# Kernel optimization log

Measured on AMD Instinct MI355X. Metric: run time of the kernel, lower is better.

Reference implementation:

```python
import jax, jax.numpy as jnp
import numpy as np

B, N, D, F, L, R = 16, 1024, 256, 128, 2, 2


def setup_inputs() -> dict:
    key = jax.random.key(0)
    ks = jax.random.split(key, 12)
    s = 0.05
    return {
        "node_embed": jax.random.normal(ks[0], (B, N, D), jnp.float32),
        "input_x": jax.random.normal(ks[1], (B, F), jnp.float32),
        "adj": jax.random.randint(ks[2], (R, B, N, N), 0, 2, jnp.int32),
        "WQi_w": jax.random.normal(ks[3], (L, F, F), jnp.float32) * s,
        "WQi_b": jnp.zeros((L, F), jnp.float32),
        "WQ_w": jax.random.normal(ks[4], (L, D + F, D), jnp.float32) * s,
        "WQ_b": jnp.zeros((L, D), jnp.float32),
        "WK_w": jax.random.normal(ks[5], (L, R, D + F, D), jnp.float32) * s,
        "WK_b": jnp.zeros((L, R, D), jnp.float32),
        "WV_w": jax.random.normal(ks[6], (L, R, D + F, D), jnp.float32) * s,
        "WV_b": jnp.zeros((L, R, D), jnp.float32),
        "WF_w": jax.random.normal(ks[7], (L, R * D, D), jnp.float32) * s,
        "WF_b": jnp.zeros((L, D), jnp.float32),
        "ln_g": jnp.ones((L, D), jnp.float32),
        "ln_b": jnp.zeros((L, D), jnp.float32),
    }


def _layer_norm(x, g, b, eps=1e-5):
    mu = jnp.mean(x, axis=-1, keepdims=True)
    var = jnp.var(x, axis=-1, keepdims=True)
    return (x - mu) * jax.lax.rsqrt(var + eps) * g + b


def reference(node_embed, input_x, adj, WQi_w, WQi_b, WQ_w, WQ_b,
              WK_w, WK_b, WV_w, WV_b, WF_w, WF_b, ln_g, ln_b):
    scale = 1.0 / (D ** 0.5)
    h = node_embed
    for l in range(L):
        # input feature projection, broadcast over nodes
        x1 = input_x @ WQi_w[l] + WQi_b[l]              # (B, F)
        x1 = jnp.broadcast_to(x1[:, None, :], (h.shape[0], h.shape[1], F))
        qc = jnp.concatenate([h, x1], axis=-1)          # (B, N, D+F)
        q = qc @ WQ_w[l] + WQ_b[l]                      # (B, N, D)
        outs = []
        for r in range(R):
            k = qc @ WK_w[l, r] + WK_b[l, r]            # (B, N, D)
            v = qc @ WV_w[l, r] + WV_b[l, r]            # (B, N, D)
            scores = jnp.einsum('bnd,bmd->bnm', q, k) * scale
            scores = jnp.where(adj[r] == 0, -1e9, scores)
            alpha = jax.nn.softmax(scores, axis=-1)
            outs.append(jnp.einsum('bnm,bmd->bnd', alpha, v))
        h_concat = jnp.concatenate(outs, axis=-1)       # (B, N, R*D)
        h_fused = jax.nn.relu(h_concat @ WF_w[l] + WF_b[l])
        h = _layer_norm(h + h_fused, ln_g[l], ln_b[l])
    return h
```

## Files before the change

### kernel.cpp

```cpp
#include <hip/hip_runtime.h>
#include <hip/hip_bf16.h>

#define BB 16
#define NN 1024
#define DD 256
#define FF_ 128
#define LL 2
#define RR 2
#define DF 384
#define MM (BB*NN)
#define NPROJ 1280
#define PK 768
#define CSC 0.09016844f

typedef __attribute__((ext_vector_type(8))) short s16x8;
typedef __attribute__((ext_vector_type(4))) float f32x4;
typedef __attribute__((ext_vector_type(16))) float f32x16;
typedef __attribute__((ext_vector_type(2))) unsigned int u32x2;
typedef __attribute__((ext_vector_type(4))) unsigned int u32x4;
typedef __attribute__((ext_vector_type(4))) unsigned short us16x4;

__device__ __forceinline__ unsigned short f2bf(float f){
  unsigned u = __builtin_bit_cast(unsigned, f);
  u += 0x7fff + ((u >> 16) & 1);
  return (unsigned short)(u >> 16);
}

__device__ __forceinline__ void gload16(const void* g, void* l){
  __builtin_amdgcn_global_load_lds(
      (const __attribute__((address_space(1))) unsigned int*)g,
      (__attribute__((address_space(3))) unsigned int*)l, 16, 0, 0);
}

#define MFMA16(a,b,c) __builtin_amdgcn_mfma_f32_16x16x32_bf16((a),(b),(c),0,0,0)
#define MFMA32(a,b,c) __builtin_amdgcn_mfma_f32_32x32x16_bf16((a),(b),(c),0,0,0)

__global__ __launch_bounds__(256) void pack_adj(const int* __restrict__ adj,
                                                unsigned long long* __restrict__ bits){
  int w = threadIdx.x >> 6, lane = threadIdx.x & 63;
  size_t row = (size_t)blockIdx.x * 4 + w;
  const int* a = adj + row * NN;
  unsigned long long* brow = bits + row * 16;
  #pragma unroll
  for (int j = 0; j < 16; ++j){
    unsigned long long m = __ballot(a[j*64 + lane] != 0);
    if (lane == 0) brow[j] = m;
  }
}

#define PREP_WT   3840
#define PREP_WTF  1024
#define PREP_BALL 10
#define PREP_X1   16
#define PREP_H    2048
#define PREP_TOT  (PREP_WT+PREP_WTF+PREP_BALL+PREP_X1+PREP_H)

__global__ __launch_bounds__(256) void prep(
    const float* __restrict__ node, const float* __restrict__ inx,
    const float* __restrict__ WQi_w, const float* __restrict__ WQi_b,
    const float* __restrict__ WQ_w, const float* __restrict__ WK_w,
    const float* __restrict__ WV_w, const float* __restrict__ WQ_b,
    const float* __restrict__ WK_b, const float* __restrict__ WV_b,
    const float* __restrict__ WF_w,
    unsigned short* __restrict__ wtall, unsigned short* __restrict__ wtf,
    float* __restrict__ ball, unsigned short* __restrict__ x1bf,
    unsigned short* __restrict__ hbf){
  int bid = blockIdx.x, t = threadIdx.x;
  if (bid < PREP_WT){
    int o = bid*256 + t;
    int l = o / (NPROJ*DF); int oo = o - l*(NPROJ*DF);
    int n = oo / DF, k = oo - n*DF;
    const float* WQ = WQ_w + (size_t)l*DF*256;
    const float* WK = WK_w + (size_t)l*RR*DF*256;
    const float* WV = WV_w + (size_t)l*RR*DF*256;
    float v;
    if (n < 256)      v = WQ[(size_t)k*256 + n] * CSC;
    else if (n < 768) v = WK[(size_t)((n-256)>>8)*(DF*256) + (size_t)k*256 + ((n-256)&255)];
    else              v = WV[(size_t)((n-768)>>8)*(DF*256) + (size_t)k*256 + ((n-768)&255)];
    wtall[o] = f2bf(v);
  } else if (bid < PREP_WT + PREP_WTF){
    int o = (bid - PREP_WT)*256 + t;
    int l = o >> 17; int oo = o & 131071;
    int n = oo >> 9, k = oo & 511;
    wtf[o] = f2bf(WF_w[(size_t)l*512*256 + (size_t)k*256 + n]);
  } else if (bid < PREP_WT + PREP_WTF + PREP_BALL){
    int o = (bid - PREP_WT - PREP_WTF)*256 + t;
    if (o < 2*NPROJ){
      int l = o / NPROJ, n = o - l*NPROJ;
      float v = (n < 256) ? WQ_b[l*256 + n] * CSC
              : (n < 768) ? WK_b[(size_t)l*512 + (n-256)]
                          : WV_b[(size_t)l*512 + (n-768)];
      ball[o] = v;
    }
  } else if (bid < PREP_WT + PREP_WTF + PREP_BALL + PREP_X1){
    int o = (bid - PREP_WT - PREP_WTF - PREP_BALL)*256 + t;
    int l = o >> 11, bj = o & 2047;
    int b = bj >> 7, j = bj & 127;
    const float* w = WQi_w + (size_t)l*FF_*FF_;
    float s = WQi_b[l*FF_ + j];
    for (int i = 0; i < FF_; ++i) s += inx[b*FF_ + i] * w[i*FF_ + j];
    x1bf[o] = f2bf(s);
  } else {
    int o = (bid - (PREP_TOT - PREP_H))*256 + t;
    const float4* src = (const float4*)node + (size_t)o*2;
    float4 a = src[0], c = src[1];
    uint4 pk;
    pk.x = (unsigned)f2bf(a.x) | ((unsigned)f2bf(a.y) << 16);
    pk.y = (unsigned)f2bf(a.z) | ((unsigned)f2bf(a.w) << 16);
    pk.z = (unsigned)f2bf(c.x) | ((unsigned)f2bf(c.y) << 16);
    pk.w = (unsigned)f2bf(c.z) | ((unsigned)f2bf(c.w) << 16);
    *(uint4*)(hbf + (size_t)o*8) = pk;
  }
}

__global__ __launch_bounds__(256) void gemm_big(const unsigned short* __restrict__ hbf,
    const unsigned short* __restrict__ x1l, const unsigned short* __restrict__ Wt,
    const float* __restrict__ bias, unsigned short* __restrict__ POUT,
    unsigned short* __restrict__ vtall){
  __shared__ unsigned short As[2][128*32];
  __shared__ unsigned short Bs[2][128*32];
  int t = threadIdx.x, lane = t & 63, w = t >> 6;
  int wr = w >> 1, wc = w & 1, l15 = lane & 15, lhi = lane >> 4;
  int bm = blockIdx.x, bn = blockIdx.y, bb = bm >> 3;
  f32x4 acc[4][4];
  #pragma unroll
  for (int m = 0; m < 4; ++m)
    #pragma unroll
    for (int n = 0; n < 4; ++n) acc[m][n] = (f32x4){0.f,0.f,0.f,0.f};

  auto STAGE = [&](int bi, int kk){
    #pragma unroll
    for (int i = 0; i < 2; ++i){
      int base = w*2048 + i*1024;
      int off = base + lane*16;
      int row = off >> 6, cb = off & 63;
      const char* asrc = (kk < 8)
        ? (const char*)hbf + ((size_t)(bm*128 + row)*256 + kk*32)*2 + cb
        : (const char*)x1l + ((size_t)bb*128 + (kk-8)*32)*2 + cb;
      gload16(asrc, (char*)As[bi] + base);
      gload16((const char*)Wt + ((size_t)(bn*128 + row)*DF + kk*32)*2 + cb,
              (char*)Bs[bi] + base);
    }
  };

  STAGE(0, 0);
  __syncthreads();
  for (int kk = 0; kk < 12; ++kk){
    int cur = kk & 1;
    if (kk + 1 < 12) STAGE(cur ^ 1, kk + 1);
    s16x8 af[4], bfr[4];
    #pragma unroll
    for (int m = 0; m < 4; ++m) af[m]  = *(const s16x8*)&As[cur][(wr*64 + m*16 + l15)*32 + lhi*8];
    #pragma unroll
    for (int n = 0; n < 4; ++n) bfr[n] = *(const s16x8*)&Bs[cur][(wc*64 + n*16 + l15)*32 + lhi*8];
    __builtin_amdgcn_s_setprio(1);
    #pragma unroll
    for (int m = 0; m < 4; ++m)
      #pragma unroll
      for (int n = 0; n < 4; ++n)
        acc[m][n] = MFMA16(af[m], bfr[n], acc[m][n]);
    __builtin_amdgcn_s_setprio(0);
    __syncthreads();
  }

  if (bn < 6){
    #pragma unroll
    for (int n = 0; n < 4; ++n){
      int gn = bn*128 + wc*64 + n*16 + l15;
      float bv = bias[gn];
      #pragma unroll
      for (int m = 0; m < 4; ++m){
        int gm = bm*128 + wr*64 + m*16 + lhi*4;
        #pragma unroll
        for (int i = 0; i < 4; ++i)
          POUT[(size_t)(gm + i)*PK + gn] = f2bf(acc[m][n][i] + bv);
      }
    }
  } else {
    #pragma unroll
    for (int n = 0; n < 4; ++n){
      int gn = bn*128 + wc*64 + n*16 + l15;
      float bv = bias[gn];
      int rv = gn - 768;
      int r = rv >> 8, d = rv & 255;
      #pragma unroll
      for (int m = 0; m < 4; ++m){
        int mb = (bm & 7)*128 + wr*64 + m*16 + lhi*4;
        us16x4 pk;
        #pragma unroll
        for (int i = 0; i < 4; ++i) pk[i] = f2bf(acc[m][n][i] + bv);
        *(us16x4*)(vtall + ((size_t)((r*16 + bb)*256 + d))*NN + mb) = pk;
      }
    }
  }
}

__global__ __launch_bounds__(512, 1) void attn10(const unsigned short* __restrict__ P,
    const unsigned short* __restrict__ VT, const unsigned long long* __restrict__ bits,
    unsigned short* __restrict__ hc){
  __shared__ char smem[147456];

  int t = threadIdx.x, lane = t & 63, w = t >> 6;
  int h = lane >> 5, l31 = lane & 31;
  int qsub = w >> 1, dh = w & 1;
  int F = blockIdx.x;
  int xcd = F & 7, j = F >> 3;
  int qt = j & 7;
  int gidx = xcd*4 + (j >> 3);
  int b = gidx & 15, r = gidx >> 4;

  size_t kcol = 256 + (size_t)r*256;
  const unsigned short* Vb = VT + ((size_t)(r*16 + b))*256*NN;
  int qrow = qt*128 + qsub*32 + l31;

  s16x8 qf[16];
  {
    const unsigned short* qp = P + ((size_t)(b*NN + qrow))*PK + h*8;
    #pragma unroll
    for (int d_ = 0; d_ < 16; ++d_) qf[d_] = *(const s16x8*)(qp + d_*16);
  }

  {
    const unsigned long long* bb0 = bits + ((size_t)(r*BB + b)*NN + qt*128)*16;
    unsigned long long* ml = (unsigned long long*)(smem + 131072);
    #pragma unroll
    for (int i = 0; i < 4; ++i){
      int idx = t + i*512;
      int kt = idx >> 7, row = idx & 127;
      ml[kt*128 + row] = bb0[(size_t)row*16 + kt];
    }
  }

  f32x16 acc[4];
  #pragma unroll
  for (int dt = 0; dt < 4; ++dt)
    #pragma unroll
    for (int i = 0; i < 16; ++i) acc[dt][i] = 0.f;
  float mrow = -3e38f, lrow = 0.f;

  auto STAGE = [&](int buf, int kt){
    char* base = smem + buf*65536;
    #pragma unroll
    for (int i = 0; i < 4; ++i){
      int o = i*8192 + t*16;
      int kr = o >> 9, cb = o & 511;
      int lcb = cb ^ ((kr & 7) << 4);
      gload16((const char*)P + ((size_t)(b*NN + kt*64 + kr)*PK + kcol)*2 + lcb,
              base + o);
    }
    #pragma unroll
    for (int i = 0; i < 4; ++i){
      int o = i*8192 + t*16;
      int vr = o >> 7, cb = o & 127;
      int lcb = cb ^ ((vr & 7) << 4);
      gload16((const char*)Vb + ((size_t)vr*NN + kt*64)*2 + lcb,
              base + 32768 + o);
    }
  };

  STAGE(0, 0);
  __syncthreads();

  for (int kt = 0; kt < 16; ++kt){
    int cur = kt & 1;
    if (kt + 1 < 16){
      STAGE(cur ^ 1, kt + 1);
      asm volatile("s_waitcnt vmcnt(8)" ::: "memory");
    } else {
      asm volatile("s_waitcnt vmcnt(0)" ::: "memory");
    }
    __builtin_amdgcn_s_barrier();
    __builtin_amdgcn_sched_barrier(0);

    unsigned long long mwv64 = *(const unsigned long long*)
        (smem + 131072 + kt*1024 + (qsub*32 + l31)*8);

    const char* Kc = smem + cur*65536;
    const char* Vc = smem + cur*65536 + 32768;

    f32x16 st0, st1;
    #pragma unroll
    for (int i = 0; i < 16; ++i){ st0[i] = 0.f; st1[i] = 0.f; }
    int swzk = (l31 & 7) << 4;
    const char* kb0 = Kc + l31*512;
    const char* kb1 = Kc + (32 + l31)*512;
    #pragma unroll
    for (int d_ = 0; d_ < 16; ++d_){
      int co = (d_*32 + h*16) ^ swzk;
      s16x8 kf0 = *(const s16x8*)(kb0 + co);
      s16x8 kf1 = *(const s16x8*)(kb1 + co);
      st0 = MFMA32(kf0, qf[d_], st0);
      st1 = MFMA32(kf1, qf[d_], st1);
    }

    auto PROC = [&](f32x16 st, unsigned mw, int vcol){
      #pragma unroll
      for (int rr = 0; rr < 16; ++rr){
        int kb = (rr & 3) + 8*(rr >> 2) + 4*h;
        st[rr] = ((mw >> kb) & 1u) ? st[rr] : -1.443e9f;
      }
      float t8[8];
      #pragma unroll
      for (int p = 0; p < 8; ++p) t8[p] = fmaxf(st[p], st[p+8]);
      #pragma unroll
      for (int p = 0; p < 4; ++p) t8[p] = fmaxf(t8[p], t8[p+4]);
      float tm = fmaxf(fmaxf(t8[0], t8[1]), fmaxf(t8[2], t8[3]));
      tm = fmaxf(tm, __shfl_xor(tm, 32));
      if (tm > mrow + 10.f){
        float f = exp2f(mrow - tm);
        mrow = tm;
        lrow *= f;
        #pragma unroll
        for (int dt = 0; dt < 4; ++dt)
          #pragma unroll
          for (int i = 0; i < 16; ++i) acc[dt][i] *= f;
      }
      #pragma unroll
      for (int rr = 0; rr < 16; ++rr) st[rr] = exp2f(st[rr] - mrow);
      #pragma unroll
      for (int p = 0; p < 8; ++p) t8[p] = st[p] + st[p+8];
      #pragma unroll
      for (int p = 0; p < 4; ++p) t8[p] = t8[p] + t8[p+4];
      float rs = (t8[0] + t8[1]) + (t8[2] + t8[3]);
      rs += __shfl_xor(rs, 32);
      lrow += rs;

      unsigned pk[8];
      #pragma unroll
      for (int p = 0; p < 8; ++p){
        unsigned rpk;
        float lo = st[p*2], hi = st[p*2+1];
        asm("v_cvt_pk_bf16_f32 %0, %1, %2" : "=v"(rpk) : "v"(lo), "v"(hi));
        pk[p] = rpk;
      }
      unsigned sA = h ? pk[0] : pk[2], sB = h ? pk[1] : pk[3];
      unsigned sC = h ? pk[4] : pk[6], sD = h ? pk[5] : pk[7];
      unsigned rxA = (unsigned)__shfl_xor((int)sA, 32);
      unsigned rxB = (unsigned)__shfl_xor((int)sB, 32);
      unsigned rxC = (unsigned)__shfl_xor((int)sC, 32);
      unsigned rxD = (unsigned)__shfl_xor((int)sD, 32);
      u32x4 pv0, pv1;
      pv0[0] = h ? rxA : pk[0]; pv0[1] = h ? rxB : pk[1];
      pv0[2] = h ? pk[2] : rxA; pv0[3] = h ? pk[3] : rxB;
      pv1[0] = h ? rxC : pk[4]; pv1[1] = h ? rxD : pk[5];
      pv1[2] = h ? pk[6] : rxC; pv1[3] = h ? pk[7] : rxD;
      s16x8 pa0 = __builtin_bit_cast(s16x8, pv0);
      s16x8 pa1 = __builtin_bit_cast(s16x8, pv1);

      #pragma unroll
      for (int dt = 0; dt < 4; ++dt){
        int vr = dh*128 + dt*32 + l31;
        int swzv = (vr & 7) << 4;
        const char* vbase = Vc + vr*128;
        s16x8 vf0 = *(const s16x8*)(vbase + ((vcol + h*16) ^ swzv));
        acc[dt] = MFMA32(vf0, pa0, acc[dt]);
        s16x8 vf1 = *(const s16x8*)(vbase + ((vcol + 32 + h*16) ^ swzv));
        acc[dt] = MFMA32(vf1, pa1, acc[dt]);
      }
    };
    PROC(st0, (unsigned)mwv64, 0);
    PROC(st1, (unsigned)(mwv64 >> 32), 64);

    __builtin_amdgcn_s_barrier();
  }

  float inv = 1.f / lrow;
  unsigned short* hrow = hc + ((size_t)(b*NN + qrow))*(RR*DD) + r*DD;
  #pragma unroll
  for (int dt = 0; dt < 4; ++dt){
    #pragma unroll
    for (int g = 0; g < 4; ++g){
      float a0 = acc[dt][g*4+0]*inv, a1 = acc[dt][g*4+1]*inv;
      float a2 = acc[dt][g*4+2]*inv, a3 = acc[dt][g*4+3]*inv;
      unsigned r0, r1;
      asm("v_cvt_pk_bf16_f32 %0, %1, %2" : "=v"(r0) : "v"(a0), "v"(a1));
      asm("v_cvt_pk_bf16_f32 %0, %1, %2" : "=v"(r1) : "v"(a2), "v"(a3));
      int d = dh*128 + dt*32 + 8*g + 4*h;
      u32x2 pv; pv[0] = r0; pv[1] = r1;
      *(u32x2*)(hrow + d) = pv;
    }
  }
}

__global__ __launch_bounds__(256) void gemm_ff(const unsigned short* __restrict__ A,
    const unsigned short* __restrict__ Wt, const float* __restrict__ bias,
    float* __restrict__ out){
  __shared__ unsigned short As[2][128*32];
  __shared__ unsigned short Bs[2][128*32];
  int t = threadIdx.x, lane = t & 63, w = t >> 6;
  int wr = w >> 1, wc = w & 1, l15 = lane & 15, lhi = lane >> 4;
  int bm = blockIdx.x, bn = blockIdx.y;
  f32x4 acc[4][4];
  #pragma unroll
  for (int m = 0; m < 4; ++m)
    #pragma unroll
    for (int n = 0; n < 4; ++n) acc[m][n] = (f32x4){0.f,0.f,0.f,0.f};

  auto STAGE = [&](int bi, int kk){
    #pragma unroll
    for (int i = 0; i < 2; ++i){
      int base = w*2048 + i*1024;
      int off = base + lane*16;
      int row = off >> 6, cb = off & 63;
      gload16((const char*)A  + ((size_t)(bm*128 + row)*512 + kk*32)*2 + cb,
              (char*)As[bi] + base);
      gload16((const char*)Wt + ((size_t)(bn*128 + row)*512 + kk*32)*2 + cb,
              (char*)Bs[bi] + base);
    }
  };

  STAGE(0, 0);
  __syncthreads();
  for (int kk = 0; kk < 16; ++kk){
    int cur = kk & 1;
    if (kk + 1 < 16) STAGE(cur ^ 1, kk + 1);
    s16x8 af[4], bfr[4];
    #pragma unroll
    for (int m = 0; m < 4; ++m) af[m]  = *(const s16x8*)&As[cur][(wr*64 + m*16 + l15)*32 + lhi*8];
    #pragma unroll
    for (int n = 0; n < 4; ++n) bfr[n] = *(const s16x8*)&Bs[cur][(wc*64 + n*16 + l15)*32 + lhi*8];
    __builtin_amdgcn_s_setprio(1);
    #pragma unroll
    for (int m = 0; m < 4; ++m)
      #pragma unroll
      for (int n = 0; n < 4; ++n)
        acc[m][n] = MFMA16(af[m], bfr[n], acc[m][n]);
    __builtin_amdgcn_s_setprio(0);
    __syncthreads();
  }

  #pragma unroll
  for (int n = 0; n < 4; ++n){
    int gn = bn*128 + wc*64 + n*16 + l15;
    float bv = bias[gn];
    #pragma unroll
    for (int m = 0; m < 4; ++m){
      int gm = bm*128 + wr*64 + m*16 + lhi*4;
      #pragma unroll
      for (int i = 0; i < 4; ++i)
        out[(size_t)(gm + i)*DD + gn] = acc[m][n][i] + bv;
    }
  }
}

template<int WRITEH>
__global__ __launch_bounds__(256) void ln_res2(const float* __restrict__ ff,
    const float* __restrict__ hin, const float* __restrict__ g,
    const float* __restrict__ bv, float* __restrict__ hout,
    unsigned short* __restrict__ hbf){
  int w = threadIdx.x >> 6, lane = threadIdx.x & 63;
  size_t row = (size_t)blockIdx.x * 4 + w;
  f32x4 fv = *(const f32x4*)(ff  + row*DD + lane*4);
  f32x4 hv = *(const f32x4*)(hin + row*DD + lane*4);
  float x[4], s = 0.f, ss = 0.f;
  #pragma unroll
  for (int j = 0; j < 4; ++j){ x[j] = fmaxf(fv[j], 0.f) + hv[j]; s += x[j]; ss += x[j]*x[j]; }
  #pragma unroll
  for (int xm = 1; xm < 64; xm <<= 1){ s += __shfl_xor(s, xm); ss += __shfl_xor(ss, xm); }
  float mu = s * (1.f/256.f);
  float var = ss * (1.f/256.f) - mu*mu;
  float rstd = rsqrtf(var + 1e-5f);
  f32x4 o;
  #pragma unroll
  for (int j = 0; j < 4; ++j){ int c = lane*4 + j; o[j] = (x[j]-mu)*rstd*g[c] + bv[c]; }
  *(f32x4*)(hout + row*DD + lane*4) = o;
  if (WRITEH){
    uint2 pv;
    pv.x = (unsigned)f2bf(o[0]) | ((unsigned)f2bf(o[1]) << 16);
    pv.y = (unsigned)f2bf(o[2]) | ((unsigned)f2bf(o[3]) << 16);
    *(uint2*)(hbf + row*DD + lane*4) = pv;
  }
}

extern "C" void kernel_launch(void* const* d_in, const int* in_sizes, int n_in,
                              void* d_out, int out_size, void* d_ws, size_t ws_size,
                              hipStream_t stream){
  (void)in_sizes; (void)n_in; (void)out_size; (void)ws_size;
  const float* node  = (const float*)d_in[0];
  const float* inx   = (const float*)d_in[1];
  const int*   adj   = (const int*)d_in[2];
  const float* WQi_w = (const float*)d_in[3];
  const float* WQi_b = (const float*)d_in[4];
  const float* WQ_w  = (const float*)d_in[5];
  const float* WQ_b  = (const float*)d_in[6];
  const float* WK_w  = (const float*)d_in[7];
  const float* WK_b  = (const float*)d_in[8];
  const float* WV_w  = (const float*)d_in[9];
  const float* WV_b  = (const float*)d_in[10];
  const float* WF_w  = (const float*)d_in[11];
  const float* WF_b  = (const float*)d_in[12];
  const float* ln_g  = (const float*)d_in[13];
  const float* ln_b  = (const float*)d_in[14];
  float* hout = (float*)d_out;

  char* wsp = (char*)d_ws;
  auto alloc = [&](size_t n){ char* p = wsp; wsp += (n + 255) & ~(size_t)255; return p; };
  unsigned long long* bits = (unsigned long long*)alloc((size_t)RR*BB*NN*16*8);
  unsigned short* wtall = (unsigned short*)alloc((size_t)2*NPROJ*DF*2);
  unsigned short* wtf   = (unsigned short*)alloc((size_t)2*DD*512*2);
  float*          ball  = (float*)alloc((size_t)2*NPROJ*4);
  unsigned short* x1bf  = (unsigned short*)alloc((size_t)2*BB*FF_*2);
  unsigned short* hbf   = (unsigned short*)alloc((size_t)MM*DD*2);
  unsigned short* POUT  = (unsigned short*)alloc((size_t)MM*PK*2);
  unsigned short* vtall = (unsigned short*)alloc((size_t)RR*BB*DD*NN*2);
  unsigned short* hc    = (unsigned short*)alloc((size_t)MM*512*2);
  float*          ffo   = (float*)alloc((size_t)MM*DD*4);

  pack_adj<<<RR*BB*NN/4, 256, 0, stream>>>(adj, bits);
  prep<<<PREP_TOT, 256, 0, stream>>>(node, inx, WQi_w, WQi_b, WQ_w, WK_w, WV_w,
                                     WQ_b, WK_b, WV_b, WF_w,
                                     wtall, wtf, ball, x1bf, hbf);

  for (int l = 0; l < LL; ++l){
    gemm_big<<<dim3(128,10), 256, 0, stream>>>(hbf, x1bf + (size_t)l*BB*FF_,
        wtall + (size_t)l*NPROJ*DF, ball + (size_t)l*NPROJ, POUT, vtall);

    attn10<<<256, 512, 0, stream>>>(POUT, vtall, bits, hc);

    gemm_ff<<<dim3(128,2), 256, 0, stream>>>(hc, wtf + (size_t)l*DD*512, WF_b + l*DD, ffo);

    if (l == 0) ln_res2<1><<<MM/4, 256, 0, stream>>>(ffo, node, ln_g, ln_b, hout, hbf);
    else        ln_res2<0><<<MM/4, 256, 0, stream>>>(ffo, (const float*)hout,
                                                     ln_g + DD, ln_b + DD, hout, nullptr);
  }
}
```

Before: 303.8 us.

## Fuse adj packing into prep, tighten GEMM waits, MFMA row-sum in attention

Folds the adjacency bit-packing kernel into the prep kernel, removing one launch. In both GEMMs, the double-buffer loop uses explicit vmcnt waits and raw barriers in place of full __syncthreads, so the next tile's loads stay in flight during compute. The attention kernel processes both 32-key halves together with a single max reduction per tile. It also computes the softmax row sum with an MFMA against a ones vector instead of VALU adds and shuffles. The hand-written waitcnt counts and barriers are fragile and could break correctness if the load count per stage changes.

Result: faster. 297.7 us (-2.0%).

```diff
diff --git a/kernel.cpp b/kernel.cpp
--- a/kernel.cpp
+++ b/kernel.cpp
@@ -35,25 +35,14 @@
 #define MFMA16(a,b,c) __builtin_amdgcn_mfma_f32_16x16x32_bf16((a),(b),(c),0,0,0)
 #define MFMA32(a,b,c) __builtin_amdgcn_mfma_f32_32x32x16_bf16((a),(b),(c),0,0,0)
 
-__global__ __launch_bounds__(256) void pack_adj(const int* __restrict__ adj,
-                                                unsigned long long* __restrict__ bits){
-  int w = threadIdx.x >> 6, lane = threadIdx.x & 63;
-  size_t row = (size_t)blockIdx.x * 4 + w;
-  const int* a = adj + row * NN;
-  unsigned long long* brow = bits + row * 16;
-  #pragma unroll
-  for (int j = 0; j < 16; ++j){
-    unsigned long long m = __ballot(a[j*64 + lane] != 0);
-    if (lane == 0) brow[j] = m;
-  }
-}
-
 #define PREP_WT   3840
 #define PREP_WTF  1024
 #define PREP_BALL 10
 #define PREP_X1   16
 #define PREP_H    2048
 #define PREP_TOT  (PREP_WT+PREP_WTF+PREP_BALL+PREP_X1+PREP_H)
+#define PREP_ADJ  8192
+#define PREP_ALL  (PREP_TOT+PREP_ADJ)
 
 __global__ __launch_bounds__(256) void prep(
     const float* __restrict__ node, const float* __restrict__ inx,
@@ -61,10 +50,10 @@
     const float* __restrict__ WQ_w, const float* __restrict__ WK_w,
     const float* __restrict__ WV_w, const float* __restrict__ WQ_b,
     const float* __restrict__ WK_b, const float* __restrict__ WV_b,
-    const float* __restrict__ WF_w,
+    const float* __restrict__ WF_w, const int* __restrict__ adj,
     unsigned short* __restrict__ wtall, unsigned short* __restrict__ wtf,
     float* __restrict__ ball, unsigned short* __restrict__ x1bf,
-    unsigned short* __restrict__ hbf){
+    unsigned short* __restrict__ hbf, unsigned long long* __restrict__ bits){
   int bid = blockIdx.x, t = threadIdx.x;
   if (bid < PREP_WT){
     int o = bid*256 + t;
@@ -100,7 +89,7 @@
     float s = WQi_b[l*FF_ + j];
     for (int i = 0; i < FF_; ++i) s += inx[b*FF_ + i] * w[i*FF_ + j];
     x1bf[o] = f2bf(s);
-  } else {
+  } else if (bid < PREP_TOT){
     int o = (bid - (PREP_TOT - PREP_H))*256 + t;
     const float4* src = (const float4*)node + (size_t)o*2;
     float4 a = src[0], c = src[1];
@@ -110,6 +99,16 @@
     pk.z = (unsigned)f2bf(c.x) | ((unsigned)f2bf(c.y) << 16);
     pk.w = (unsigned)f2bf(c.z) | ((unsigned)f2bf(c.w) << 16);
     *(uint4*)(hbf + (size_t)o*8) = pk;
+  } else {
+    int w = t >> 6, lane = t & 63;
+    size_t row = (size_t)(bid - PREP_TOT) * 4 + w;
+    const int* a = adj + row * NN;
+    unsigned long long* brow = bits + row * 16;
+    #pragma unroll
+    for (int j = 0; j < 16; ++j){
+      unsigned long long m = __ballot(a[j*64 + lane] != 0);
+      if (lane == 0) brow[j] = m;
+    }
   }
 }
 
@@ -144,10 +143,16 @@
   };
 
   STAGE(0, 0);
-  __syncthreads();
   for (int kk = 0; kk < 12; ++kk){
     int cur = kk & 1;
-    if (kk + 1 < 12) STAGE(cur ^ 1, kk + 1);
+    if (kk + 1 < 12){
+      STAGE(cur ^ 1, kk + 1);
+      asm volatile("s_waitcnt vmcnt(4)" ::: "memory");
+    } else {
+      asm volatile("s_waitcnt vmcnt(0)" ::: "memory");
+    }
+    __builtin_amdgcn_s_barrier();
+    __builtin_amdgcn_sched_barrier(0);
     s16x8 af[4], bfr[4];
     #pragma unroll
     for (int m = 0; m < 4; ++m) af[m]  = *(const s16x8*)&As[cur][(wr*64 + m*16 + l15)*32 + lhi*8];
@@ -160,7 +165,7 @@
       for (int n = 0; n < 4; ++n)
         acc[m][n] = MFMA16(af[m], bfr[n], acc[m][n]);
     __builtin_amdgcn_s_setprio(0);
-    __syncthreads();
+    __builtin_amdgcn_s_barrier();
   }
 
   if (bn < 6){
@@ -195,7 +200,7 @@
   }
 }
 
-__global__ __launch_bounds__(512, 1) void attn10(const unsigned short* __restrict__ P,
+__global__ __launch_bounds__(512, 1) void attn11(const unsigned short* __restrict__ P,
     const unsigned short* __restrict__ VT, const unsigned long long* __restrict__ bits,
     unsigned short* __restrict__ hc){
   __shared__ char smem[147456];
@@ -231,12 +236,19 @@
     }
   }
 
+  s16x8 ones;
+  #pragma unroll
+  for (int i = 0; i < 8; ++i) ones[i] = (short)0x3F80;
+
   f32x16 acc[4];
   #pragma unroll
   for (int dt = 0; dt < 4; ++dt)
     #pragma unroll
     for (int i = 0; i < 16; ++i) acc[dt][i] = 0.f;
-  float mrow = -3e38f, lrow = 0.f;
+  f32x16 accl;
+  #pragma unroll
+  for (int i = 0; i < 16; ++i) accl[i] = 0.f;
+  float mrow = -3e38f;
 
   auto STAGE = [&](int buf, int kt){
     char* base = smem + buf*65536;
@@ -284,6 +296,7 @@
     int swzk = (l31 & 7) << 4;
     const char* kb0 = Kc + l31*512;
     const char* kb1 = Kc + (32 + l31)*512;
+    __builtin_amdgcn_s_setprio(1);
     #pragma unroll
     for (int d_ = 0; d_ < 16; ++d_){
       int co = (d_*32 + h*16) ^ swzk;
@@ -292,79 +305,106 @@
       st0 = MFMA32(kf0, qf[d_], st0);
       st1 = MFMA32(kf1, qf[d_], st1);
     }
-
-    auto PROC = [&](f32x16 st, unsigned mw, int vcol){
+    __builtin_amdgcn_s_setprio(0);
+
+    unsigned mw0 = (unsigned)mwv64 >> (h*4);
+    unsigned mw1 = (unsigned)(mwv64 >> 32) >> (h*4);
+    #pragma unroll
+    for (int rr = 0; rr < 16; ++rr){
+      const int kb = (rr & 3) + 8*(rr >> 2);
+      st0[rr] = ((mw0 >> kb) & 1u) ? st0[rr] : -1.443e9f;
+      st1[rr] = ((mw1 >> kb) & 1u) ? st1[rr] : -1.443e9f;
+    }
+    float t8[8];
+    #pragma unroll
+    for (int p = 0; p < 8; ++p) t8[p] = fmaxf(fmaxf(st0[p], st0[p+8]),
+                                              fmaxf(st1[p], st1[p+8]));
+    #pragma unroll
+    for (int p = 0; p < 4; ++p) t8[p] = fmaxf(t8[p], t8[p+4]);
+    float tm = fmaxf(fmaxf(t8[0], t8[1]), fmaxf(t8[2], t8[3]));
+    tm = fmaxf(tm, __shfl_xor(tm, 32));
+    if (tm > mrow + 10.f){
+      float f = exp2f(mrow - tm);
+      mrow = tm;
+      accl[0] *= f;
       #pragma unroll
-      for (int rr = 0; rr < 16; ++rr){
-        int kb = (rr & 3) + 8*(rr >> 2) + 4*h;
-        st[rr] = ((mw >> kb) & 1u) ? st[rr] : -1.443e9f;
-      }
-      float t8[8];
-      #pragma unroll
-      for (int p = 0; p < 8; ++p) t8[p] = fmaxf(st[p], st[p+8]);
-      #pragma unroll
-      for (int p = 0; p < 4; ++p) t8[p] = fmaxf(t8[p], t8[p+4]);
-      float tm = fmaxf(fmaxf(t8[0], t8[1]), fmaxf(t8[2], t8[3]));
-      tm = fmaxf(tm, __shfl_xor(tm, 32));
-      if (tm > mrow + 10.f){
-        float f = exp2f(mrow - tm);
-        mrow = tm;
-        lrow *= f;
+      for (int dt = 0; dt < 4; ++dt)
         #pragma unroll
-        for (int dt = 0; dt < 4; ++dt)
-          #pragma unroll
-          for (int i = 0; i < 16; ++i) acc[dt][i] *= f;
-      }
-      #pragma unroll
-      for (int rr = 0; rr < 16; ++rr) st[rr] = exp2f(st[rr] - mrow);
-      #pragma unroll
-      for (int p = 0; p < 8; ++p) t8[p] = st[p] + st[p+8];
-      #pragma unroll
-      for (int p = 0; p < 4; ++p) t8[p] = t8[p] + t8[p+4];
-      float rs = (t8[0] + t8[1]) + (t8[2] + t8[3]);
-      rs += __shfl_xor(rs, 32);
-      lrow += rs;
-
-      unsigned pk[8];
-      #pragma unroll
-      for (int p = 0; p < 8; ++p){
-        unsigned rpk;
-        float lo = st[p*2], hi = st[p*2+1];
-        asm("v_cvt_pk_bf16_f32 %0, %1, %2" : "=v"(rpk) : "v"(lo), "v"(hi));
-        pk[p] = rpk;
-      }
-      unsigned sA = h ? pk[0] : pk[2], sB = h ? pk[1] : pk[3];
-      unsigned sC = h ? pk[4] : pk[6], sD = h ? pk[5] : pk[7];
+        for (int i = 0; i < 16; ++i) acc[dt][i] *= f;
+    }
+    #pragma unroll
+    for (int rr = 0; rr < 16; ++rr){
+      st0[rr] = exp2f(st0[rr] - mrow);
+      st1[rr] = exp2f(st1[rr] - mrow);
+    }
+
+    unsigned pk0[8], pk1[8];
+    #pragma unroll
+    for (int p = 0; p < 8; ++p){
+      unsigned r0, r1;
+      float a0 = st0[p*2], a1 = st0[p*2+1];
+      float b0 = st1[p*2], b1 = st1[p*2+1];
+      asm("v_cvt_pk_bf16_f32 %0, %1, %2" : "=v"(r0) : "v"(a0), "v"(a1));
+      asm("v_cvt_pk_bf16_f32 %0, %1, %2" : "=v"(r1) : "v"(b0), "v"(b1));
+      pk0[p] = r0; pk1[p] = r1;
+    }
+    s16x8 pa00, pa01, pa10, pa11;
+    {
+      unsigned sA = h ? pk0[0] : pk0[2], sB = h ? pk0[1] : pk0[3];
+      unsigned sC = h ? pk0[4] : pk0[6], sD = h ? pk0[5] : pk0[7];
       unsigned rxA = (unsigned)__shfl_xor((int)sA, 32);
       unsigned rxB = (unsigned)__shfl_xor((int)sB, 32);
       unsigned rxC = (unsigned)__shfl_xor((int)sC, 32);
       unsigned rxD = (unsigned)__shfl_xor((int)sD, 32);
-      u32x4 pv0, pv1;
-      pv0[0] = h ? rxA : pk[0]; pv0[1] = h ? rxB : pk[1];
-      pv0[2] = h ? pk[2] : rxA; pv0[3] = h ? pk[3] : rxB;
-      pv1[0] = h ? rxC : pk[4]; pv1[1] = h ? rxD : pk[5];
-      pv1[2] = h ? pk[6] : rxC; pv1[3] = h ? pk[7] : rxD;
-      s16x8 pa0 = __builtin_bit_cast(s16x8, pv0);
-      s16x8 pa1 = __builtin_bit_cast(s16x8, pv1);
-
-      #pragma unroll
-      for (int dt = 0; dt < 4; ++dt){
-        int vr = dh*128 + dt*32 + l31;
-        int swzv = (vr & 7) << 4;
-        const char* vbase = Vc + vr*128;
-        s16x8 vf0 = *(const s16x8*)(vbase + ((vcol + h*16) ^ swzv));
-        acc[dt] = MFMA32(vf0, pa0, acc[dt]);
-        s16x8 vf1 = *(const s16x8*)(vbase + ((vcol + 32 + h*16) ^ swzv));
-        acc[dt] = MFMA32(vf1, pa1, acc[dt]);
-      }
-    };
-    PROC(st0, (unsigned)mwv64, 0);
-    PROC(st1, (unsigned)(mwv64 >> 32), 64);
+      u32x4 v0, v1;
+      v0[0] = h ? rxA : pk0[0]; v0[1] = h ? rxB : pk0[1];
+      v0[2] = h ? pk0[2] : rxA; v0[3] = h ? pk0[3] : rxB;
+      v1[0] = h ? rxC : pk0[4]; v1[1] = h ? rxD : pk0[5];
+      v1[2] = h ? pk0[6] : rxC; v1[3] = h ? pk0[7] : rxD;
+      pa00 = __builtin_bit_cast(s16x8, v0);
+      pa01 = __builtin_bit_cast(s16x8, v1);
+    }
+    {
+      unsigned sA = h ? pk1[0] : pk1[2], sB = h ? pk1[1] : pk1[3];
+      unsigned sC = h ? pk1[4] : pk1[6], sD = h ? pk1[5] : pk1[7];
+      unsigned rxA = (unsigned)__shfl_xor((int)sA, 32);
+      unsigned rxB = (unsigned)__shfl_xor((int)sB, 32);
+      unsigned rxC = (unsigned)__shfl_xor((int)sC, 32);
+      unsigned rxD = (unsigned)__shfl_xor((int)sD, 32);
+      u32x4 v0, v1;
+      v0[0] = h ? rxA : pk1[0]; v0[1] = h ? rxB : pk1[1];
+      v0[2] = h ? pk1[2] : rxA; v0[3] = h ? pk1[3] : rxB;
+      v1[0] = h ? rxC : pk1[4]; v1[1] = h ? rxD : pk1[5];
+      v1[2] = h ? pk1[6] : rxC; v1[3] = h ? pk1[7] : rxD;
+      pa10 = __builtin_bit_cast(s16x8, v0);
+      pa11 = __builtin_bit_cast(s16x8, v1);
+    }
+
+    __builtin_amdgcn_s_setprio(1);
+    accl = MFMA32(ones, pa00, accl);
+    accl = MFMA32(ones, pa01, accl);
+    accl = MFMA32(ones, pa10, accl);
+    accl = MFMA32(ones, pa11, accl);
+    #pragma unroll
+    for (int dt = 0; dt < 4; ++dt){
+      int vr = dh*128 + dt*32 + l31;
+      int swzv = (vr & 7) << 4;
+      const char* vbase = Vc + vr*128;
+      s16x8 vf0 = *(const s16x8*)(vbase + ((h*16) ^ swzv));
+      acc[dt] = MFMA32(vf0, pa00, acc[dt]);
+      s16x8 vf1 = *(const s16x8*)(vbase + ((32 + h*16) ^ swzv));
+      acc[dt] = MFMA32(vf1, pa01, acc[dt]);
+      s16x8 vf2 = *(const s16x8*)(vbase + ((64 + h*16) ^ swzv));
+      acc[dt] = MFMA32(vf2, pa10, acc[dt]);
+      s16x8 vf3 = *(const s16x8*)(vbase + ((96 + h*16) ^ swzv));
+      acc[dt] = MFMA32(vf3, pa11, acc[dt]);
+    }
+    __builtin_amdgcn_s_setprio(0);
 
     __builtin_amdgcn_s_barrier();
   }
 
-  float inv = 1.f / lrow;
+  float inv = 1.f / accl[0];
   unsigned short* hrow = hc + ((size_t)(b*NN + qrow))*(RR*DD) + r*DD;
   #pragma unroll
   for (int dt = 0; dt < 4; ++dt){
@@ -410,10 +450,16 @@
   };
 
   STAGE(0, 0);
-  __syncthreads();
   for (int kk = 0; kk < 16; ++kk){
     int cur = kk & 1;
-    if (kk + 1 < 16) STAGE(cur ^ 1, kk + 1);
+    if (kk + 1 < 16){
+      STAGE(cur ^ 1, kk + 1);
+      asm volatile("s_waitcnt vmcnt(4)" ::: "memory");
+    } else {
+      asm volatile("s_waitcnt vmcnt(0)" ::: "memory");
+    }
+    __builtin_amdgcn_s_barrier();
+    __builtin_amdgcn_sched_barrier(0);
     s16x8 af[4], bfr[4];
     #pragma unroll
     for (int m = 0; m < 4; ++m) af[m]  = *(const s16x8*)&As[cur][(wr*64 + m*16 + l15)*32 + lhi*8];
@@ -426,7 +472,7 @@
       for (int n = 0; n < 4; ++n)
         acc[m][n] = MFMA16(af[m], bfr[n], acc[m][n]);
     __builtin_amdgcn_s_setprio(0);
-    __syncthreads();
+    __builtin_amdgcn_s_barrier();
   }
 
   #pragma unroll
@@ -506,16 +552,15 @@
   unsigned short* hc    = (unsigned short*)alloc((size_t)MM*512*2);
   float*          ffo   = (float*)alloc((size_t)MM*DD*4);
 
-  pack_adj<<<RR*BB*NN/4, 256, 0, stream>>>(adj, bits);
-  prep<<<PREP_TOT, 256, 0, stream>>>(node, inx, WQi_w, WQi_b, WQ_w, WK_w, WV_w,
-                                     WQ_b, WK_b, WV_b, WF_w,
-                                     wtall, wtf, ball, x1bf, hbf);
+  prep<<<PREP_ALL, 256, 0, stream>>>(node, inx, WQi_w, WQi_b, WQ_w, WK_w, WV_w,
+                                     WQ_b, WK_b, WV_b, WF_w, adj,
+                                     wtall, wtf, ball, x1bf, hbf, bits);
 
   for (int l = 0; l < LL; ++l){
     gemm_big<<<dim3(128,10), 256, 0, stream>>>(hbf, x1bf + (size_t)l*BB*FF_,
         wtall + (size_t)l*NPROJ*DF, ball + (size_t)l*NPROJ, POUT, vtall);
 
-    attn10<<<256, 512, 0, stream>>>(POUT, vtall, bits, hc);
+    attn11<<<256, 512, 0, stream>>>(POUT, vtall, bits, hc);
 
     gemm_ff<<<dim3(128,2), 256, 0, stream>>>(hc, wtf + (size_t)l*DD*512, WF_b + l*DD, ffo);
 
```

## Fuse adjacency packing into prep, relax GEMM barriers, reswizzle attention LDS

Applied to the files above, without the earlier changes.

The adjacency bit-packing kernel is merged into the prep kernel as extra blocks, which saves one launch. Both GEMM loops replace __syncthreads with explicit s_waitcnt vmcnt plus raw s_barrier, so the next tile's global-to-LDS loads can stay in flight while the current tile is computed. The attention kernel changes its LDS XOR swizzles for K (wider row mask) and V (rows paired into 256-byte lines) to reduce bank conflicts. The hand-written vmcnt counts rely on each thread issuing exactly four loads per stage; if the compiler reorders memory ops, that assumption could break correctness.

Measured after the change: 297.1 us. -2.2%, faster.

```diff
diff --git a/kernel.cpp b/kernel.cpp
--- a/kernel.cpp
+++ b/kernel.cpp
@@ -35,25 +35,14 @@
 #define MFMA16(a,b,c) __builtin_amdgcn_mfma_f32_16x16x32_bf16((a),(b),(c),0,0,0)
 #define MFMA32(a,b,c) __builtin_amdgcn_mfma_f32_32x32x16_bf16((a),(b),(c),0,0,0)
 
-__global__ __launch_bounds__(256) void pack_adj(const int* __restrict__ adj,
-                                                unsigned long long* __restrict__ bits){
-  int w = threadIdx.x >> 6, lane = threadIdx.x & 63;
-  size_t row = (size_t)blockIdx.x * 4 + w;
-  const int* a = adj + row * NN;
-  unsigned long long* brow = bits + row * 16;
-  #pragma unroll
-  for (int j = 0; j < 16; ++j){
-    unsigned long long m = __ballot(a[j*64 + lane] != 0);
-    if (lane == 0) brow[j] = m;
-  }
-}
-
 #define PREP_WT   3840
 #define PREP_WTF  1024
 #define PREP_BALL 10
 #define PREP_X1   16
 #define PREP_H    2048
 #define PREP_TOT  (PREP_WT+PREP_WTF+PREP_BALL+PREP_X1+PREP_H)
+#define PREP_ADJ  8192
+#define PREP_ALL  (PREP_TOT+PREP_ADJ)
 
 __global__ __launch_bounds__(256) void prep(
     const float* __restrict__ node, const float* __restrict__ inx,
@@ -61,10 +50,10 @@
     const float* __restrict__ WQ_w, const float* __restrict__ WK_w,
     const float* __restrict__ WV_w, const float* __restrict__ WQ_b,
     const float* __restrict__ WK_b, const float* __restrict__ WV_b,
-    const float* __restrict__ WF_w,
+    const float* __restrict__ WF_w, const int* __restrict__ adj,
     unsigned short* __restrict__ wtall, unsigned short* __restrict__ wtf,
     float* __restrict__ ball, unsigned short* __restrict__ x1bf,
-    unsigned short* __restrict__ hbf){
+    unsigned short* __restrict__ hbf, unsigned long long* __restrict__ bits){
   int bid = blockIdx.x, t = threadIdx.x;
   if (bid < PREP_WT){
     int o = bid*256 + t;
@@ -100,7 +89,7 @@
     float s = WQi_b[l*FF_ + j];
     for (int i = 0; i < FF_; ++i) s += inx[b*FF_ + i] * w[i*FF_ + j];
     x1bf[o] = f2bf(s);
-  } else {
+  } else if (bid < PREP_TOT){
     int o = (bid - (PREP_TOT - PREP_H))*256 + t;
     const float4* src = (const float4*)node + (size_t)o*2;
     float4 a = src[0], c = src[1];
@@ -110,6 +99,16 @@
     pk.z = (unsigned)f2bf(c.x) | ((unsigned)f2bf(c.y) << 16);
     pk.w = (unsigned)f2bf(c.z) | ((unsigned)f2bf(c.w) << 16);
     *(uint4*)(hbf + (size_t)o*8) = pk;
+  } else {
+    int w = t >> 6, lane = t & 63;
+    size_t row = (size_t)(bid - PREP_TOT) * 4 + w;
+    const int* a = adj + row * NN;
+    unsigned long long* brow = bits + row * 16;
+    #pragma unroll
+    for (int j = 0; j < 16; ++j){
+      unsigned long long m = __ballot(a[j*64 + lane] != 0);
+      if (lane == 0) brow[j] = m;
+    }
   }
 }
 
@@ -144,10 +143,16 @@
   };
 
   STAGE(0, 0);
-  __syncthreads();
   for (int kk = 0; kk < 12; ++kk){
     int cur = kk & 1;
-    if (kk + 1 < 12) STAGE(cur ^ 1, kk + 1);
+    if (kk + 1 < 12){
+      STAGE(cur ^ 1, kk + 1);
+      asm volatile("s_waitcnt vmcnt(4)" ::: "memory");
+    } else {
+      asm volatile("s_waitcnt vmcnt(0)" ::: "memory");
+    }
+    __builtin_amdgcn_s_barrier();
+    __builtin_amdgcn_sched_barrier(0);
     s16x8 af[4], bfr[4];
     #pragma unroll
     for (int m = 0; m < 4; ++m) af[m]  = *(const s16x8*)&As[cur][(wr*64 + m*16 + l15)*32 + lhi*8];
@@ -160,7 +165,7 @@
       for (int n = 0; n < 4; ++n)
         acc[m][n] = MFMA16(af[m], bfr[n], acc[m][n]);
     __builtin_amdgcn_s_setprio(0);
-    __syncthreads();
+    __builtin_amdgcn_s_barrier();
   }
 
   if (bn < 6){
@@ -195,7 +200,7 @@
   }
 }
 
-__global__ __launch_bounds__(512, 1) void attn10(const unsigned short* __restrict__ P,
+__global__ __launch_bounds__(512, 1) void attn12(const unsigned short* __restrict__ P,
     const unsigned short* __restrict__ VT, const unsigned long long* __restrict__ bits,
     unsigned short* __restrict__ hc){
   __shared__ char smem[147456];
@@ -244,16 +249,17 @@
     for (int i = 0; i < 4; ++i){
       int o = i*8192 + t*16;
       int kr = o >> 9, cb = o & 511;
-      int lcb = cb ^ ((kr & 7) << 4);
+      int lcb = cb ^ ((kr & 31) << 4);
       gload16((const char*)P + ((size_t)(b*NN + kt*64 + kr)*PK + kcol)*2 + lcb,
               base + o);
     }
     #pragma unroll
     for (int i = 0; i < 4; ++i){
       int o = i*8192 + t*16;
-      int vr = o >> 7, cb = o & 127;
-      int lcb = cb ^ ((vr & 7) << 4);
-      gload16((const char*)Vb + ((size_t)vr*NN + kt*64)*2 + lcb,
+      int p = o >> 8, rem = o & 255;
+      int lrem = rem ^ ((p & 15) << 4);
+      int drow = p + (lrem >> 7)*128, col = lrem & 127;
+      gload16((const char*)Vb + ((size_t)drow*NN + kt*64)*2 + col,
               base + 32768 + o);
     }
   };
@@ -281,7 +287,7 @@
     f32x16 st0, st1;
     #pragma unroll
     for (int i = 0; i < 16; ++i){ st0[i] = 0.f; st1[i] = 0.f; }
-    int swzk = (l31 & 7) << 4;
+    int swzk = l31 << 4;
     const char* kb0 = Kc + l31*512;
     const char* kb1 = Kc + (32 + l31)*512;
     #pragma unroll
@@ -349,12 +355,12 @@
 
       #pragma unroll
       for (int dt = 0; dt < 4; ++dt){
-        int vr = dh*128 + dt*32 + l31;
-        int swzv = (vr & 7) << 4;
-        const char* vbase = Vc + vr*128;
-        s16x8 vf0 = *(const s16x8*)(vbase + ((vcol + h*16) ^ swzv));
+        int p = dt*32 + l31;
+        int swzv = (p & 15) << 4;
+        const char* vbase = Vc + p*256;
+        s16x8 vf0 = *(const s16x8*)(vbase + ((dh*128 + vcol + h*16) ^ swzv));
         acc[dt] = MFMA32(vf0, pa0, acc[dt]);
-        s16x8 vf1 = *(const s16x8*)(vbase + ((vcol + 32 + h*16) ^ swzv));
+        s16x8 vf1 = *(const s16x8*)(vbase + ((dh*128 + vcol + 32 + h*16) ^ swzv));
         acc[dt] = MFMA32(vf1, pa1, acc[dt]);
       }
     };
@@ -410,10 +416,16 @@
   };
 
   STAGE(0, 0);
-  __syncthreads();
   for (int kk = 0; kk < 16; ++kk){
     int cur = kk & 1;
-    if (kk + 1 < 16) STAGE(cur ^ 1, kk + 1);
+    if (kk + 1 < 16){
+      STAGE(cur ^ 1, kk + 1);
+      asm volatile("s_waitcnt vmcnt(4)" ::: "memory");
+    } else {
+      asm volatile("s_waitcnt vmcnt(0)" ::: "memory");
+    }
+    __builtin_amdgcn_s_barrier();
+    __builtin_amdgcn_sched_barrier(0);
     s16x8 af[4], bfr[4];
     #pragma unroll
     for (int m = 0; m < 4; ++m) af[m]  = *(const s16x8*)&As[cur][(wr*64 + m*16 + l15)*32 + lhi*8];
@@ -426,7 +438,7 @@
       for (int n = 0; n < 4; ++n)
         acc[m][n] = MFMA16(af[m], bfr[n], acc[m][n]);
     __builtin_amdgcn_s_setprio(0);
-    __syncthreads();
+    __builtin_amdgcn_s_barrier();
   }
 
   #pragma unroll
@@ -506,16 +518,15 @@
   unsigned short* hc    = (unsigned short*)alloc((size_t)MM*512*2);
   float*          ffo   = (float*)alloc((size_t)MM*DD*4);
 
-  pack_adj<<<RR*BB*NN/4, 256, 0, stream>>>(adj, bits);
-  prep<<<PREP_TOT, 256, 0, stream>>>(node, inx, WQi_w, WQi_b, WQ_w, WK_w, WV_w,
-                                     WQ_b, WK_b, WV_b, WF_w,
-                                     wtall, wtf, ball, x1bf, hbf);
+  prep<<<PREP_ALL, 256, 0, stream>>>(node, inx, WQi_w, WQi_b, WQ_w, WK_w, WV_w,
+                                     WQ_b, WK_b, WV_b, WF_w, adj,
+                                     wtall, wtf, ball, x1bf, hbf, bits);
 
   for (int l = 0; l < LL; ++l){
     gemm_big<<<dim3(128,10), 256, 0, stream>>>(hbf, x1bf + (size_t)l*BB*FF_,
         wtall + (size_t)l*NPROJ*DF, ball + (size_t)l*NPROJ, POUT, vtall);
 
-    attn10<<<256, 512, 0, stream>>>(POUT, vtall, bits, hc);
+    attn12<<<256, 512, 0, stream>>>(POUT, vtall, bits, hc);
 
     gemm_ff<<<dim3(128,2), 256, 0, stream>>>(hc, wtf + (size_t)l*DD*512, WF_b + l*DD, ffo);
 
```
